# Performance work log

Hardware: AMD Instinct MI355X
Metric: run time of the kernel (lower is better)

Reference implementation:

```python
import jax, jax.numpy as jnp
import numpy as np

NEG_SLOPE = 0.2

def gat_conv(x, W, a_src, a_dst, b, src, dst, n_nodes):
    # x: [N, F_in], W: [F_in, F_out], a_src/a_dst: [F_out], b: [F_out]
    h = x @ W                                   # [N, F_out]
    alpha_s = h @ a_src                         # [N]
    alpha_d = h @ a_dst                         # [N]
    e = jax.nn.leaky_relu(alpha_s[src] + alpha_d[dst], NEG_SLOPE)  # [E]
    # scatter-softmax over incoming edges of each dst node
    m = jax.ops.segment_max(e, dst, num_segments=n_nodes)
    m = jnp.where(jnp.isfinite(m), m, 0.0)      # nodes with no in-edges
    p = jnp.exp(e - m[dst])
    denom = jax.ops.segment_sum(p, dst, num_segments=n_nodes)
    alpha = p / (denom[dst] + 1e-16)            # [E]
    out = jax.ops.segment_sum(alpha[:, None] * h[src], dst, num_segments=n_nodes)
    return out + b

def setup_inputs() -> dict:
    key = jax.random.key(0)
    N, E, F_IN, H, C = 100000, 1600000, 128, 64, 2
    ks = jax.random.split(key, 10)
    x = jax.random.normal(ks[0], (N, F_IN), dtype=jnp.float32)
    edge_index = jax.random.randint(ks[1], (2, E), 0, N, dtype=jnp.int64)
    s1 = 1.0 / np.sqrt(F_IN)
    s2 = 1.0 / np.sqrt(H)
    return {
        "x": x,
        "edge_index": edge_index,
        "W1": jax.random.normal(ks[2], (F_IN, H), dtype=jnp.float32) * s1,
        "a_src1": jax.random.normal(ks[3], (H,), dtype=jnp.float32) * s2,
        "a_dst1": jax.random.normal(ks[4], (H,), dtype=jnp.float32) * s2,
        "b1": jnp.zeros((H,), dtype=jnp.float32),
        "W2": jax.random.normal(ks[5], (H, C), dtype=jnp.float32) * s2,
        "a_src2": jax.random.normal(ks[6], (C,), dtype=jnp.float32),
        "a_dst2": jax.random.normal(ks[7], (C,), dtype=jnp.float32),
        "b2": jnp.zeros((C,), dtype=jnp.float32),
    }

def reference(x, edge_index, W1, a_src1, a_dst1, b1, W2, a_src2, a_dst2, b2):
    N = x.shape[0]
    loops = jnp.arange(N, dtype=edge_index.dtype)   # GATConv add_self_loops=True
    src = jnp.concatenate([edge_index[0], loops])
    dst = jnp.concatenate([edge_index[1], loops])
    h = gat_conv(x, W1, a_src1, a_dst1, b1, src, dst, N)
    h = jax.nn.relu(h)
    # F.dropout with training=False is identity (eval mode)
    out = gat_conv(h, W2, a_src2, a_dst2, b2, src, dst, N)
    return out
```

## Files before the change

### kernel.cpp

```cpp
#include <hip/hip_runtime.h>
#include <math.h>

constexpr int N_NODES = 100000;
constexpr int N_EDGES = 1600000;
constexpr int F_IN    = 128;
constexpr int F_H     = 64;
constexpr float NEG_SLOPE = 0.2f;

constexpr int NBUCK  = (N_NODES + 255) / 256;
constexpr int BUFCAP = 6144;
constexpr int LCAP   = 6144;
constexpr int CPAD   = 16;

constexpr int SB   = 256;
constexpr int EPT  = 4;
constexpr int EPR  = 256 * EPT;
constexpr int G    = 16;
constexpr int BCAP = 32;
constexpr int BSTR = 33;

constexpr int GEMM_BLOCKS = (N_NODES + 63) / 64;

__device__ inline float lrelu(float v) { return v > 0.f ? v : NEG_SLOPE * v; }
__device__ inline float blo(unsigned u) { return __uint_as_float(u << 16); }
__device__ inline float bhi(unsigned u) { return __uint_as_float(u & 0xFFFF0000u); }
__device__ inline unsigned bf16hi(float f) {
    unsigned u = __float_as_uint(f);
    return (u + 0x7FFFu + ((u >> 16) & 1u)) & 0xFFFF0000u;
}
__device__ inline unsigned bf16lo(float f) {
    unsigned u = __float_as_uint(f);
    return (u + 0x7FFFu + ((u >> 16) & 1u)) >> 16;
}

__global__ __launch_bounds__(256) void k_gemm1_bucketize(
    const float* __restrict__ x, const float* __restrict__ W1,
    const float* __restrict__ a_s, const float* __restrict__ a_d,
    unsigned* __restrict__ h1b, float* __restrict__ as1, float* __restrict__ ad1,
    const int* __restrict__ ei, int* __restrict__ gcur, unsigned* __restrict__ buf)
{
    __shared__ union SM {
        struct { unsigned bin_buf[NBUCK][BSTR]; int bin_cnt[NBUCK]; } bk;
        struct { float vsP[4][64]; float vdP[4][64]; } gm;
    } sm;

    const int t = threadIdx.x;

    if (blockIdx.x < SB) {
        for (int i = t; i < NBUCK; i += 256) sm.bk.bin_cnt[i] = 0;
        __syncthreads();

        const int per = N_EDGES / SB;
        const int e0 = blockIdx.x * per;
        const int e1 = (blockIdx.x == SB - 1) ? N_EDGES : (e0 + per);

        int cs[EPT], cd[EPT];
#pragma unroll
        for (int q = 0; q < EPT; ++q) {
            const int i = e0 + q * 256 + t;
            cs[q] = (i < e1) ? ei[i] : -1;
            cd[q] = (i < e1) ? ei[N_EDGES + i] : 0;
        }

        for (int base = e0; base < e1; base += EPR) {
            int ls[EPT], ld[EPT];
#pragma unroll
            for (int q = 0; q < EPT; ++q) { ls[q] = cs[q]; ld[q] = cd[q]; }
            const int nbase = base + EPR;
            if (nbase < e1) {
#pragma unroll
                for (int q = 0; q < EPT; ++q) {
                    const int i = nbase + q * 256 + t;
                    cs[q] = (i < e1) ? ei[i] : -1;
                    cd[q] = (i < e1) ? ei[N_EDGES + i] : 0;
                }
            }
#pragma unroll
            for (int q = 0; q < EPT; ++q) {
                if (ls[q] >= 0) {
                    const int b = ld[q] >> 8;
                    const int pos = atomicAdd(&sm.bk.bin_cnt[b], 1);
                    if (pos < BCAP)
                        sm.bk.bin_buf[b][pos] = ((unsigned)ls[q] << 8) | (unsigned)(ld[q] & 255);
                }
            }
            __syncthreads();
            for (int bb = t; bb < NBUCK; bb += 256) {
                const int cnt = sm.bk.bin_cnt[bb];
                if (cnt >= G) {
                    const int take = cnt & ~(G - 1);
                    const int gbase = atomicAdd(&gcur[bb * CPAD], take);
                    if (gbase + take <= BUFCAP) {
                        unsigned* __restrict__ dst = buf + (size_t)bb * BUFCAP + gbase;
                        const int src0 = cnt - take;
                        for (int u = 0; u < take; u += 4) {
                            uint4 v;
                            v.x = sm.bk.bin_buf[bb][src0 + u];
                            v.y = sm.bk.bin_buf[bb][src0 + u + 1];
                            v.z = sm.bk.bin_buf[bb][src0 + u + 2];
                            v.w = sm.bk.bin_buf[bb][src0 + u + 3];
                            *(uint4*)(dst + u) = v;
                        }
                    }
                    sm.bk.bin_cnt[bb] = cnt - take;
                }
            }
            __syncthreads();
        }
        for (int bb = t; bb < NBUCK; bb += 256) {
            const int cnt = sm.bk.bin_cnt[bb];
            if (cnt > 0) {
                const int gbase = atomicAdd(&gcur[bb * CPAD], cnt);
                if (gbase + cnt <= BUFCAP) {
                    unsigned* __restrict__ dst = buf + (size_t)bb * BUFCAP + gbase;
                    for (int u = 0; u < cnt; ++u) dst[u] = sm.bk.bin_buf[bb][u];
                }
            }
        }
        return;
    }

    const int lane = t & 63;
    const int w    = __builtin_amdgcn_readfirstlane(t >> 6);
    const int fo   = w * 16;
    const int row  = (blockIdx.x - SB) * 64 + lane;
    const bool valid = row < N_NODES;

    float acc[16];
#pragma unroll
    for (int i = 0; i < 16; ++i) acc[i] = 0.f;

    if (valid) {
        const float4* __restrict__ xr = (const float4*)(x + (size_t)row * F_IN);
        float4 xv = xr[0];
        for (int k4 = 0; k4 < F_IN / 4; ++k4) {
            const float4 xn = xr[(k4 + 1) & (F_IN / 4 - 1)];
            const float* __restrict__ wk = W1 + (size_t)k4 * 4 * F_H + fo;
#pragma unroll
            for (int kk = 0; kk < 4; ++kk) {
                const float xs = (kk == 0) ? xv.x : (kk == 1) ? xv.y : (kk == 2) ? xv.z : xv.w;
                const float* __restrict__ ws = wk + kk * F_H;
#pragma unroll
                for (int i = 0; i < 16; ++i)
                    acc[i] = fmaf(xs, ws[i], acc[i]);
            }
            xv = xn;
        }
    }

    float vs = 0.f, vd = 0.f;
#pragma unroll
    for (int i = 0; i < 16; ++i) {
        vs = fmaf(acc[i], a_s[fo + i], vs);
        vd = fmaf(acc[i], a_d[fo + i], vd);
    }
    sm.gm.vsP[w][lane] = vs;
    sm.gm.vdP[w][lane] = vd;
    __syncthreads();
    if (w == 0 && valid) {
        as1[row] = sm.gm.vsP[0][lane] + sm.gm.vsP[1][lane] + sm.gm.vsP[2][lane] + sm.gm.vsP[3][lane];
        ad1[row] = sm.gm.vdP[0][lane] + sm.gm.vdP[1][lane] + sm.gm.vdP[2][lane] + sm.gm.vdP[3][lane];
    }

    if (valid) {
        unsigned up[8];
#pragma unroll
        for (int i = 0; i < 8; ++i)
            up[i] = bf16lo(acc[2 * i]) | bf16hi(acc[2 * i + 1]);
        uint4* __restrict__ hr = (uint4*)(h1b + (size_t)row * 32 + w * 8);
        hr[0] = make_uint4(up[0], up[1], up[2], up[3]);
        hr[1] = make_uint4(up[4], up[5], up[6], up[7]);
    }
}

__global__ __launch_bounds__(1024) void k_csr_build(
    const int* __restrict__ gcur, const unsigned* __restrict__ buf,
    int* __restrict__ row_start, int* __restrict__ csr)
{
    __shared__ int lcsr[LCAP];
    __shared__ int hist[256];
    __shared__ int lstart[257];
    __shared__ int lcur[256];
    __shared__ int redsm[16];
    __shared__ int gb_sm;

    const int b  = blockIdx.x;
    const int t  = threadIdx.x;
    const int nd = min(256, N_NODES - (b << 8));
    const int m  = min(gcur[b * CPAD], BUFCAP);
    const unsigned* __restrict__ sb = buf + (size_t)b * BUFCAP;

    int part = 0;
    for (int i = t; i < b; i += 1024) part += min(gcur[i * CPAD], BUFCAP);
#pragma unroll
    for (int o = 32; o; o >>= 1) part += __shfl_xor(part, o, 64);
    if ((t & 63) == 0) redsm[t >> 6] = part;
    if (t < 256) hist[t] = 0;
    __syncthreads();
    if (t == 0) {
        int s = 0;
#pragma unroll
        for (int i = 0; i < 16; ++i) s += redsm[i];
        gb_sm = s;
    }
    __syncthreads();

    for (int i = t; i < m; i += 1024) atomicAdd(&hist[sb[i] & 255], 1);
    __syncthreads();

    for (int o = 1; o < 256; o <<= 1) {
        int a = 0;
        if (t < 256 && t >= o) a = hist[t - o];
        __syncthreads();
        if (t < 256) hist[t] += a;
        __syncthreads();
    }
    if (t < 256) { lstart[t + 1] = hist[t]; lcur[t] = 0; }
    if (t == 0) lstart[0] = 0;
    __syncthreads();

    for (int i = t; i < m; i += 1024) {
        const unsigned v = sb[i];
        const int dl = v & 255;
        const int p  = atomicAdd(&lcur[dl], 1);
        const int pp = lstart[dl] + p;
        if (pp < LCAP) lcsr[pp] = (int)(v >> 8);
    }
    __syncthreads();

    const int gb   = gb_sm;
    const int mtot = lstart[256];
    for (int i = t; i < mtot; i += 1024) csr[gb + i] = lcsr[i];
    if (t < nd) row_start[(b << 8) + t + 1] = gb + lstart[t + 1];
    if (b == 0 && t == 0) row_start[0] = 0;
}

__global__ __launch_bounds__(256, 4) void k_agg1(
    const int* __restrict__ row_start, const int* __restrict__ csr,
    const float* __restrict__ as1, const float* __restrict__ ad1,
    const unsigned* __restrict__ h1b,
    const float* __restrict__ b1, const float* __restrict__ W2,
    const float* __restrict__ a_s2, const float* __restrict__ a_d2,
    float* __restrict__ h2, float* __restrict__ as2, float* __restrict__ ad2)
{
    const int n = blockIdx.x * 4 + (threadIdx.x >> 6);
    const int j = threadIdx.x & 63;
    if (n >= N_NODES) return;

    const int g  = j >> 3;
    const int oq = (j & 7) << 2;

    const int r0  = row_start[n];
    const int deg = row_start[n + 1] - r0;
    const float ad = ad1[n];

    float acc0[8], acc1[8];
#pragma unroll
    for (int i = 0; i < 8; ++i) { acc0[i] = 0.f; acc1[i] = 0.f; }
    float den_l = 0.f;

#define FMA8(ACC, P, U)                                            \
    ACC[0] = fmaf(P, blo(U.x), ACC[0]); ACC[1] = fmaf(P, bhi(U.x), ACC[1]); \
    ACC[2] = fmaf(P, blo(U.y), ACC[2]); ACC[3] = fmaf(P, bhi(U.y), ACC[3]); \
    ACC[4] = fmaf(P, blo(U.z), ACC[4]); ACC[5] = fmaf(P, bhi(U.z), ACC[5]); \
    ACC[6] = fmaf(P, blo(U.w), ACC[6]); ACC[7] = fmaf(P, bhi(U.w), ACC[7]);
#define LD8(S) (*(const uint4*)(h1b + ((size_t)(S) << 5) + oq))

    if (deg <= 63) {
        int sj = n;
        if (j < deg) sj = csr[r0 + j];
        const float aj = as1[sj];
        const int s0 = __shfl(sj, g,      64);
        const int s1 = __shfl(sj, 8 + g,  64);
        const uint4 u0 = LD8(s0);
        const uint4 u1 = LD8(s1);
        float pj = 0.f;
        if (j <= deg) pj = __expf(lrelu(aj + ad));
        den_l = pj;
        const float p0 = __shfl(pj, g,      64);
        const float p1 = __shfl(pj, 8 + g,  64);

        const int tot = deg + 1;
        const bool t16 = tot > 16, t24 = tot > 24, t32 = tot > 32;
        int s2, s3; uint4 u2, u3; float p2, p3;
        if (t16) { s2 = __shfl(sj, 16 + g, 64); u2 = LD8(s2); p2 = __shfl(pj, 16 + g, 64); }
        if (t24) { s3 = __shfl(sj, 24 + g, 64); u3 = LD8(s3); p3 = __shfl(pj, 24 + g, 64); }
        FMA8(acc0, p0, u0) FMA8(acc1, p1, u1)
        if (t16) { FMA8(acc0, p2, u2) }
        if (t24) { FMA8(acc1, p3, u3) }
        if (t32) {
            for (int base = 32; base < tot; base += 8) {
                const int   sA = __shfl(sj, base + g, 64);
                const float pA = __shfl(pj, base + g, 64);
                const uint4 ua = LD8(sA);
                FMA8(acc0, pA, ua)
            }
        }
    } else {
        {
            const float ps = __expf(lrelu(as1[n] + ad));
            if (j == 0) den_l += ps;
            if (g == 0) {
                const uint4 uv = LD8(n);
                FMA8(acc0, ps, uv)
            }
        }
        for (int cb = r0; cb < r0 + deg; cb += 64) {
            const int cnt = min(64, r0 + deg - cb);
            int sj = 0; float pj = 0.f;
            if (j < cnt) { sj = csr[cb + j]; pj = __expf(lrelu(as1[sj] + ad)); }
            den_l += pj;
            for (int base = 0; base < cnt; base += 16) {
                const int   sA = __shfl(sj, base + g, 64);
                const float pA = __shfl(pj, base + g, 64);
                const uint4 ua = LD8(sA);
                FMA8(acc0, pA, ua)
                if (base + 8 < cnt) {
                    const int   sB = __shfl(sj, base + 8 + g, 64);
                    const float pB = __shfl(pj, base + 8 + g, 64);
                    const uint4 ub = LD8(sB);
                    FMA8(acc1, pB, ub)
                }
            }
        }
    }
#undef FMA8
#undef LD8

    float den = den_l;
#pragma unroll
    for (int o = 32; o; o >>= 1) den += __shfl_xor(den, o, 64);

#pragma unroll
    for (int i = 0; i < 8; ++i) acc0[i] += acc1[i];
#pragma unroll
    for (int o = 8; o <= 32; o <<= 1) {
#pragma unroll
        for (int i = 0; i < 8; ++i) acc0[i] += __shfl_xor(acc0[i], o, 64);
    }

    const float inv = 1.f / (den + 1e-16f);
    const int ob = (j & 7) << 3;
    const float4 b0 = *(const float4*)(b1 + ob);
    const float4 b4 = *(const float4*)(b1 + ob + 4);
    float v[8];
    v[0] = acc0[0] * inv + b0.x; v[1] = acc0[1] * inv + b0.y;
    v[2] = acc0[2] * inv + b0.z; v[3] = acc0[3] * inv + b0.w;
    v[4] = acc0[4] * inv + b4.x; v[5] = acc0[5] * inv + b4.y;
    v[6] = acc0[6] * inv + b4.z; v[7] = acc0[7] * inv + b4.w;
#pragma unroll
    for (int i = 0; i < 8; ++i) v[i] = v[i] > 0.f ? v[i] : 0.f;

    const float4* __restrict__ wq = (const float4*)(W2 + 2 * ob);
    const float4 w0 = wq[0], w1 = wq[1], w2 = wq[2], w3 = wq[3];
    float c0 = v[0] * w0.x + v[1] * w0.z + v[2] * w1.x + v[3] * w1.z
             + v[4] * w2.x + v[5] * w2.z + v[6] * w3.x + v[7] * w3.z;
    float c1 = v[0] * w0.y + v[1] * w0.w + v[2] * w1.y + v[3] * w1.w
             + v[4] * w2.y + v[5] * w2.w + v[6] * w3.y + v[7] * w3.w;
#pragma unroll
    for (int o = 1; o <= 4; o <<= 1) {
        c0 += __shfl_xor(c0, o, 64);
        c1 += __shfl_xor(c1, o, 64);
    }
    if (j == 0) {
        h2[n * 2 + 0] = c0;
        h2[n * 2 + 1] = c1;
        as2[n] = c0 * a_s2[0] + c1 * a_s2[1];
        ad2[n] = c0 * a_d2[0] + c1 * a_d2[1];
    }
}

__global__ __launch_bounds__(256) void k_agg2_wave(
    const int* __restrict__ row_start, const int* __restrict__ csr,
    const float* __restrict__ as2, const float* __restrict__ ad2,
    const float* __restrict__ h2, const float* __restrict__ b2,
    float* __restrict__ out)
{
    const int n = blockIdx.x * 4 + (threadIdx.x >> 6);
    const int j = threadIdx.x & 63;
    if (n >= N_NODES) return;
    const int r0  = row_start[n];
    const int deg = row_start[n + 1] - r0;
    const float ad = ad2[n];
    const float2* __restrict__ h22 = (const float2*)h2;

    float den_l = 0.f, x0 = 0.f, x1 = 0.f;
    if (deg <= 63) {
        int sj = n;
        if (j < deg) sj = csr[r0 + j];
        const float  aj = as2[sj];
        const float2 hv = h22[sj];
        float p = 0.f;
        if (j <= deg) p = __expf(lrelu(aj + ad));
        den_l = p; x0 = p * hv.x; x1 = p * hv.y;
    } else {
        if (j == 0) {
            const float p = __expf(lrelu(as2[n] + ad));
            const float2 hv = h22[n];
            den_l = p; x0 = p * hv.x; x1 = p * hv.y;
        }
        for (int idx = r0 + j; idx < r0 + deg; idx += 64) {
            const int s = csr[idx];
            const float p = __expf(lrelu(as2[s] + ad));
            const float2 hv = h22[s];
            den_l += p; x0 = fmaf(p, hv.x, x0); x1 = fmaf(p, hv.y, x1);
        }
    }
#pragma unroll
    for (int o = 32; o; o >>= 1) {
        den_l += __shfl_xor(den_l, o, 64);
        x0    += __shfl_xor(x0, o, 64);
        x1    += __shfl_xor(x1, o, 64);
    }
    if (j == 0) {
        const float inv = 1.f / (den_l + 1e-16f);
        out[n * 2 + 0] = x0 * inv + b2[0];
        out[n * 2 + 1] = x1 * inv + b2[1];
    }
}

extern "C" void kernel_launch(void* const* d_in, const int* in_sizes, int n_in,
                              void* d_out, int out_size, void* d_ws, size_t ws_size,
                              hipStream_t stream)
{
    const float* x    = (const float*)d_in[0];
    const int*   ei   = (const int*)d_in[1];
    const float* W1   = (const float*)d_in[2];
    const float* as1w = (const float*)d_in[3];
    const float* ad1w = (const float*)d_in[4];
    const float* b1   = (const float*)d_in[5];
    const float* W2   = (const float*)d_in[6];
    const float* as2w = (const float*)d_in[7];
    const float* ad2w = (const float*)d_in[8];
    const float* b2   = (const float*)d_in[9];
    float* out = (float*)d_out;

    float* ws = (float*)d_ws;
    size_t off = 0;
    unsigned* h1b = (unsigned*)(ws + off); off += (size_t)N_NODES * 32;
    float* as1 = ws + off; off += N_NODES;
    float* ad1 = ws + off; off += N_NODES;
    float* h2  = ws + off; off += (size_t)N_NODES * 2;
    float* as2 = ws + off; off += N_NODES;
    float* ad2 = ws + off; off += N_NODES;
    int* gcur      = (int*)(ws + off); off += NBUCK * CPAD;
    unsigned* buf  = (unsigned*)(ws + off); off += (size_t)NBUCK * BUFCAP;
    int* row_start = (int*)(ws + off); off += N_NODES + 1;
    int* csr       = (int*)(ws + off); off += N_EDGES;

    hipMemsetAsync(gcur, 0, NBUCK * CPAD * sizeof(int), stream);

    k_gemm1_bucketize <<<SB + GEMM_BLOCKS, 256, 0, stream>>>(
        x, W1, as1w, ad1w, h1b, as1, ad1, ei, gcur, buf);
    k_csr_build       <<<NBUCK, 1024, 0, stream>>>(gcur, buf, row_start, csr);
    k_agg1            <<<(N_NODES + 3) / 4, 256, 0, stream>>>(
        row_start, csr, as1, ad1, h1b, b1, W2, as2w, ad2w, h2, as2, ad2);
    k_agg2_wave       <<<(N_NODES + 3) / 4, 256, 0, stream>>>(row_start, csr, as2, ad2, h2, b2, out);
}
```

Measured before the change: 236.0 us.

## Fuse CSR build with layer-1 aggregation using shared-memory CSR

Merges the CSR construction kernel and the first-layer attention aggregation into a single kernel per 256-node bucket. After building the local CSR in shared memory, each of 16 waves processes 16 nodes, reading neighbor lists from LDS instead of global csr/row_start. This removes a kernel launch and a global CSR read for layer 1. In exchange, only 391 blocks of 1024 threads do the aggregation with large LDS use, which may reduce occupancy and parallelism compared with the separate 25k-block aggregation kernel.

```diff
diff --git a/kernel.cpp b/kernel.cpp
--- a/kernel.cpp
+++ b/kernel.cpp
@@ -173,9 +173,14 @@
     }
 }
 
-__global__ __launch_bounds__(1024) void k_csr_build(
+__global__ __launch_bounds__(1024) void k_csr_agg1(
     const int* __restrict__ gcur, const unsigned* __restrict__ buf,
-    int* __restrict__ row_start, int* __restrict__ csr)
+    int* __restrict__ row_start, int* __restrict__ csr,
+    const float* __restrict__ as1, const float* __restrict__ ad1,
+    const unsigned* __restrict__ h1b,
+    const float* __restrict__ b1, const float* __restrict__ W2,
+    const float* __restrict__ a_s2, const float* __restrict__ a_d2,
+    float* __restrict__ h2, float* __restrict__ as2, float* __restrict__ ad2)
 {
     __shared__ int lcsr[LCAP];
     __shared__ int hist[256];
@@ -233,31 +238,12 @@
     for (int i = t; i < mtot; i += 1024) csr[gb + i] = lcsr[i];
     if (t < nd) row_start[(b << 8) + t + 1] = gb + lstart[t + 1];
     if (b == 0 && t == 0) row_start[0] = 0;
-}
-
-__global__ __launch_bounds__(256, 4) void k_agg1(
-    const int* __restrict__ row_start, const int* __restrict__ csr,
-    const float* __restrict__ as1, const float* __restrict__ ad1,
-    const unsigned* __restrict__ h1b,
-    const float* __restrict__ b1, const float* __restrict__ W2,
-    const float* __restrict__ a_s2, const float* __restrict__ a_d2,
-    float* __restrict__ h2, float* __restrict__ as2, float* __restrict__ ad2)
-{
-    const int n = blockIdx.x * 4 + (threadIdx.x >> 6);
-    const int j = threadIdx.x & 63;
-    if (n >= N_NODES) return;
-
-    const int g  = j >> 3;
-    const int oq = (j & 7) << 2;
-
-    const int r0  = row_start[n];
-    const int deg = row_start[n + 1] - r0;
-    const float ad = ad1[n];
-
-    float acc0[8], acc1[8];
-#pragma unroll
-    for (int i = 0; i < 8; ++i) { acc0[i] = 0.f; acc1[i] = 0.f; }
-    float den_l = 0.f;
+    __syncthreads();
+
+    const int w16 = t >> 6;
+    const int j   = t & 63;
+    const int g   = j >> 3;
+    const int oq  = (j & 7) << 2;
 
 #define FMA8(ACC, P, U)                                            \
     ACC[0] = fmaf(P, blo(U.x), ACC[0]); ACC[1] = fmaf(P, bhi(U.x), ACC[1]); \
@@ -266,108 +252,122 @@
     ACC[6] = fmaf(P, blo(U.w), ACC[6]); ACC[7] = fmaf(P, bhi(U.w), ACC[7]);
 #define LD8(S) (*(const uint4*)(h1b + ((size_t)(S) << 5) + oq))
 
-    if (deg <= 63) {
-        int sj = n;
-        if (j < deg) sj = csr[r0 + j];
-        const float aj = as1[sj];
-        const int s0 = __shfl(sj, g,      64);
-        const int s1 = __shfl(sj, 8 + g,  64);
-        const uint4 u0 = LD8(s0);
-        const uint4 u1 = LD8(s1);
-        float pj = 0.f;
-        if (j <= deg) pj = __expf(lrelu(aj + ad));
-        den_l = pj;
-        const float p0 = __shfl(pj, g,      64);
-        const float p1 = __shfl(pj, 8 + g,  64);
-
-        const int tot = deg + 1;
-        const bool t16 = tot > 16, t24 = tot > 24, t32 = tot > 32;
-        int s2, s3; uint4 u2, u3; float p2, p3;
-        if (t16) { s2 = __shfl(sj, 16 + g, 64); u2 = LD8(s2); p2 = __shfl(pj, 16 + g, 64); }
-        if (t24) { s3 = __shfl(sj, 24 + g, 64); u3 = LD8(s3); p3 = __shfl(pj, 24 + g, 64); }
-        FMA8(acc0, p0, u0) FMA8(acc1, p1, u1)
-        if (t16) { FMA8(acc0, p2, u2) }
-        if (t24) { FMA8(acc1, p3, u3) }
-        if (t32) {
-            for (int base = 32; base < tot; base += 8) {
-                const int   sA = __shfl(sj, base + g, 64);
-                const float pA = __shfl(pj, base + g, 64);
-                const uint4 ua = LD8(sA);
-                FMA8(acc0, pA, ua)
-            }
-        }
-    } else {
-        {
-            const float ps = __expf(lrelu(as1[n] + ad));
-            if (j == 0) den_l += ps;
-            if (g == 0) {
-                const uint4 uv = LD8(n);
-                FMA8(acc0, ps, uv)
-            }
-        }
-        for (int cb = r0; cb < r0 + deg; cb += 64) {
-            const int cnt = min(64, r0 + deg - cb);
-            int sj = 0; float pj = 0.f;
-            if (j < cnt) { sj = csr[cb + j]; pj = __expf(lrelu(as1[sj] + ad)); }
-            den_l += pj;
-            for (int base = 0; base < cnt; base += 16) {
-                const int   sA = __shfl(sj, base + g, 64);
-                const float pA = __shfl(pj, base + g, 64);
-                const uint4 ua = LD8(sA);
-                FMA8(acc0, pA, ua)
-                if (base + 8 < cnt) {
-                    const int   sB = __shfl(sj, base + 8 + g, 64);
-                    const float pB = __shfl(pj, base + 8 + g, 64);
-                    const uint4 ub = LD8(sB);
-                    FMA8(acc1, pB, ub)
-                }
-            }
+    for (int k = 0; k < 16; ++k) {
+        const int ln = w16 * 16 + k;
+        if (ln >= nd) break;
+        const int n   = (b << 8) + ln;
+        const int r0  = lstart[ln];
+        const int deg = lstart[ln + 1] - r0;
+        const float ad = ad1[n];
+
+        float acc0[8], acc1[8];
+#pragma unroll
+        for (int i = 0; i < 8; ++i) { acc0[i] = 0.f; acc1[i] = 0.f; }
+        float den_l = 0.f;
+
+        if (deg <= 63) {
+            int sj = n;
+            if (j < deg) sj = lcsr[r0 + j];
+            const float aj = as1[sj];
+            const int s0 = __shfl(sj, g,      64);
+            const int s1 = __shfl(sj, 8 + g,  64);
+            const uint4 u0 = LD8(s0);
+            const uint4 u1 = LD8(s1);
+            float pj = 0.f;
+            if (j <= deg) pj = __expf(lrelu(aj + ad));
+            den_l = pj;
+            const float p0 = __shfl(pj, g,      64);
+            const float p1 = __shfl(pj, 8 + g,  64);
+
+            const int tot = deg + 1;
+            const bool t16c = tot > 16, t24c = tot > 24, t32c = tot > 32;
+            int s2, s3; uint4 u2, u3; float p2, p3;
+            if (t16c) { s2 = __shfl(sj, 16 + g, 64); u2 = LD8(s2); p2 = __shfl(pj, 16 + g, 64); }
+            if (t24c) { s3 = __shfl(sj, 24 + g, 64); u3 = LD8(s3); p3 = __shfl(pj, 24 + g, 64); }
+            FMA8(acc0, p0, u0) FMA8(acc1, p1, u1)
+            if (t16c) { FMA8(acc0, p2, u2) }
+            if (t24c) { FMA8(acc1, p3, u3) }
+            if (t32c) {
+                for (int base = 32; base < tot; base += 8) {
+                    const int   sA = __shfl(sj, base + g, 64);
+                    const float pA = __shfl(pj, base + g, 64);
+                    const uint4 ua = LD8(sA);
+                    FMA8(acc0, pA, ua)
+                }
+            }
+        } else {
+            {
+                const float ps = __expf(lrelu(as1[n] + ad));
+                if (j == 0) den_l += ps;
+                if (g == 0) {
+                    const uint4 uv = LD8(n);
+                    FMA8(acc0, ps, uv)
+                }
+            }
+            for (int cb = 0; cb < deg; cb += 64) {
+                const int cnt = min(64, deg - cb);
+                int sj = 0; float pj = 0.f;
+                if (j < cnt) { sj = lcsr[r0 + cb + j]; pj = __expf(lrelu(as1[sj] + ad)); }
+                den_l += pj;
+                for (int base = 0; base < cnt; base += 16) {
+                    const int   sA = __shfl(sj, base + g, 64);
+                    const float pA = __shfl(pj, base + g, 64);
+                    const uint4 ua = LD8(sA);
+                    FMA8(acc0, pA, ua)
+                    if (base + 8 < cnt) {
+                        const int   sB = __shfl(sj, base + 8 + g, 64);
+                        const float pB = __shfl(pj, base + 8 + g, 64);
+                        const uint4 ub = LD8(sB);
+                        FMA8(acc1, pB, ub)
+                    }
+                }
+            }
+        }
+
+        float den = den_l;
+#pragma unroll
+        for (int o = 32; o; o >>= 1) den += __shfl_xor(den, o, 64);
+
+#pragma unroll
+        for (int i = 0; i < 8; ++i) acc0[i] += acc1[i];
+#pragma unroll
+        for (int o = 8; o <= 32; o <<= 1) {
+#pragma unroll
+            for (int i = 0; i < 8; ++i) acc0[i] += __shfl_xor(acc0[i], o, 64);
+        }
+
+        const float inv = 1.f / (den + 1e-16f);
+        const int ob = (j & 7) << 3;
+        const float4 b0 = *(const float4*)(b1 + ob);
+        const float4 b4 = *(const float4*)(b1 + ob + 4);
+        float v[8];
+        v[0] = acc0[0] * inv + b0.x; v[1] = acc0[1] * inv + b0.y;
+        v[2] = acc0[2] * inv + b0.z; v[3] = acc0[3] * inv + b0.w;
+        v[4] = acc0[4] * inv + b4.x; v[5] = acc0[5] * inv + b4.y;
+        v[6] = acc0[6] * inv + b4.z; v[7] = acc0[7] * inv + b4.w;
+#pragma unroll
+        for (int i = 0; i < 8; ++i) v[i] = v[i] > 0.f ? v[i] : 0.f;
+
+        const float4* __restrict__ wq = (const float4*)(W2 + 2 * ob);
+        const float4 w0 = wq[0], w1 = wq[1], w2 = wq[2], w3 = wq[3];
+        float c0 = v[0] * w0.x + v[1] * w0.z + v[2] * w1.x + v[3] * w1.z
+                 + v[4] * w2.x + v[5] * w2.z + v[6] * w3.x + v[7] * w3.z;
+        float c1 = v[0] * w0.y + v[1] * w0.w + v[2] * w1.y + v[3] * w1.w
+                 + v[4] * w2.y + v[5] * w2.w + v[6] * w3.y + v[7] * w3.w;
+#pragma unroll
+        for (int o = 1; o <= 4; o <<= 1) {
+            c0 += __shfl_xor(c0, o, 64);
+            c1 += __shfl_xor(c1, o, 64);
+        }
+        if (j == 0) {
+            h2[n * 2 + 0] = c0;
+            h2[n * 2 + 1] = c1;
+            as2[n] = c0 * a_s2[0] + c1 * a_s2[1];
+            ad2[n] = c0 * a_d2[0] + c1 * a_d2[1];
         }
     }
 #undef FMA8
 #undef LD8
-
-    float den = den_l;
-#pragma unroll
-    for (int o = 32; o; o >>= 1) den += __shfl_xor(den, o, 64);
-
-#pragma unroll
-    for (int i = 0; i < 8; ++i) acc0[i] += acc1[i];
-#pragma unroll
-    for (int o = 8; o <= 32; o <<= 1) {
-#pragma unroll
-        for (int i = 0; i < 8; ++i) acc0[i] += __shfl_xor(acc0[i], o, 64);
-    }
-
-    const float inv = 1.f / (den + 1e-16f);
-    const int ob = (j & 7) << 3;
-    const float4 b0 = *(const float4*)(b1 + ob);
-    const float4 b4 = *(const float4*)(b1 + ob + 4);
-    float v[8];
-    v[0] = acc0[0] * inv + b0.x; v[1] = acc0[1] * inv + b0.y;
-    v[2] = acc0[2] * inv + b0.z; v[3] = acc0[3] * inv + b0.w;
-    v[4] = acc0[4] * inv + b4.x; v[5] = acc0[5] * inv + b4.y;
-    v[6] = acc0[6] * inv + b4.z; v[7] = acc0[7] * inv + b4.w;
-#pragma unroll
-    for (int i = 0; i < 8; ++i) v[i] = v[i] > 0.f ? v[i] : 0.f;
-
-    const float4* __restrict__ wq = (const float4*)(W2 + 2 * ob);
-    const float4 w0 = wq[0], w1 = wq[1], w2 = wq[2], w3 = wq[3];
-    float c0 = v[0] * w0.x + v[1] * w0.z + v[2] * w1.x + v[3] * w1.z
-             + v[4] * w2.x + v[5] * w2.z + v[6] * w3.x + v[7] * w3.z;
-    float c1 = v[0] * w0.y + v[1] * w0.w + v[2] * w1.y + v[3] * w1.w
-             + v[4] * w2.y + v[5] * w2.w + v[6] * w3.y + v[7] * w3.w;
-#pragma unroll
-    for (int o = 1; o <= 4; o <<= 1) {
-        c0 += __shfl_xor(c0, o, 64);
-        c1 += __shfl_xor(c1, o, 64);
-    }
-    if (j == 0) {
-        h2[n * 2 + 0] = c0;
-        h2[n * 2 + 1] = c1;
-        as2[n] = c0 * a_s2[0] + c1 * a_s2[1];
-        ad2[n] = c0 * a_d2[0] + c1 * a_d2[1];
-    }
 }
 
 __global__ __launch_bounds__(256) void k_agg2_wave(
@@ -452,8 +452,7 @@
 
     k_gemm1_bucketize <<<SB + GEMM_BLOCKS, 256, 0, stream>>>(
         x, W1, as1w, ad1w, h1b, as1, ad1, ei, gcur, buf);
-    k_csr_build       <<<NBUCK, 1024, 0, stream>>>(gcur, buf, row_start, csr);
-    k_agg1            <<<(N_NODES + 3) / 4, 256, 0, stream>>>(
-        row_start, csr, as1, ad1, h1b, b1, W2, as2w, ad2w, h2, as2, ad2);
+    k_csr_agg1        <<<NBUCK, 1024, 0, stream>>>(
+        gcur, buf, row_start, csr, as1, ad1, h1b, b1, W2, as2w, ad2w, h2, as2, ad2);
     k_agg2_wave       <<<(N_NODES + 3) / 4, 256, 0, stream>>>(row_start, csr, as2, ad2, h2, b2, out);
 }
```

Result: slower. 253.9 us (+7.6%).
